# Kernel tuning notes

Hardware: AMD Instinct MI355X
Metric: run time of the kernel (lower is better)

Reference implementation:

```python
import jax, jax.numpy as jnp
import numpy as np

N_NODES = 100000
N_EDGES = 1600000
N_GRAPHS = 64
IN_CH = 128
HID = 128
N_CLASSES = 8


def setup_inputs() -> dict:
    key = jax.random.key(0)
    ks = jax.random.split(key, 8)
    x = jax.random.normal(ks[0], (N_NODES, IN_CH), dtype=jnp.float32)
    edge_index = jax.random.randint(ks[1], (2, N_EDGES), 0, N_NODES, dtype=jnp.int64)
    batch = jnp.sort(jax.random.randint(ks[2], (N_NODES,), 0, N_GRAPHS, dtype=jnp.int64))
    s1 = 1.0 / np.sqrt(IN_CH)
    s2 = 1.0 / np.sqrt(HID)
    W1 = jax.random.normal(ks[3], (IN_CH, HID), dtype=jnp.float32) * s1
    b1 = jnp.zeros((HID,), dtype=jnp.float32)
    W2 = jax.random.normal(ks[4], (HID, HID), dtype=jnp.float32) * s2
    b2 = jnp.zeros((HID,), dtype=jnp.float32)
    lin_W = jax.random.normal(ks[5], (HID, N_CLASSES), dtype=jnp.float32) * s2
    lin_b = jnp.zeros((N_CLASSES,), dtype=jnp.float32)
    return {"x": x, "edge_index": edge_index, "batch": batch,
            "W1": W1, "b1": b1, "W2": W2, "b2": b2,
            "lin_W": lin_W, "lin_b": lin_b}


def _gcn_norm(edge_index, n_nodes):
    # add self-loops, compute symmetric normalization coefficients
    loops = jnp.arange(n_nodes, dtype=edge_index.dtype)
    src = jnp.concatenate([edge_index[0], loops])
    dst = jnp.concatenate([edge_index[1], loops])
    ones = jnp.ones(src.shape[0], dtype=jnp.float32)
    deg = jax.ops.segment_sum(ones, dst, num_segments=n_nodes)
    dinv = jnp.where(deg > 0, jax.lax.rsqrt(jnp.maximum(deg, 1.0)), 0.0)
    norm = dinv[src] * dinv[dst]  # [E + N]
    return src, dst, norm


def _gcn_conv(x, W, b, src, dst, norm, n_nodes):
    xw = x @ W                               # [N, H]
    msg = xw[src] * norm[:, None]            # gather + scale, [E+N, H]
    out = jax.ops.segment_sum(msg, dst, num_segments=n_nodes)
    return out + b


def reference(x, edge_index, batch, W1, b1, W2, b2, lin_W, lin_b):
    n = x.shape[0]
    src, dst, norm = _gcn_norm(edge_index, n)
    h = jax.nn.relu(_gcn_conv(x, W1, b1, src, dst, norm, n))
    h = _gcn_conv(h, W2, b2, src, dst, norm, n)
    # global mean pool over graphs
    sums = jax.ops.segment_sum(h, batch, num_segments=N_GRAPHS)
    cnts = jax.ops.segment_sum(jnp.ones(n, dtype=h.dtype), batch, num_segments=N_GRAPHS)
    pooled = sums / jnp.maximum(cnts, 1.0)[:, None]
    return pooled @ lin_W + lin_b
```

## Files before the change

kernel.cpp:

```cpp
#include <hip/hip_runtime.h>
#include <hip/hip_fp16.h>
#include <cstdint>
#include <cstddef>

#define NNODES 100000
#define NEDGES 1600000
#define NGRAPHS 64
#define BSHIFT 7
#define BRANGE 128
#define NB 782
#define CAP 4096
#define NZ NB
#define LP 136
#define NAB 25000

typedef short short8v __attribute__((ext_vector_type(8)));
typedef float float4v __attribute__((ext_vector_type(4)));
typedef float float2v __attribute__((ext_vector_type(2)));

__device__ inline short f2h_s(float f) {
    __half h = __float2half(f);
    return __builtin_bit_cast(short, h);
}
__device__ inline ushort f2h_u(float f) {
    __half h = __float2half(f);
    return __builtin_bit_cast(ushort, h);
}
__device__ inline uint h22u(__half2 h) { return __builtin_bit_cast(uint, h); }

__device__ inline float2v fp8x2_f32(uint u) {
    return __builtin_amdgcn_cvt_pk_f32_fp8((int)u, false);
}
__device__ inline ushort f32_fp8x2(float a, float b) {
    return (ushort)__builtin_amdgcn_cvt_pk_fp8_f32(a, b, 0, false);
}


__global__ __launch_bounds__(256) void k_setup(int* __restrict__ zb,
                                               const float* __restrict__ W1,
                                               const float* __restrict__ W2,
                                               short8v* __restrict__ o1,
                                               short8v* __restrict__ o2,
                                               uint* __restrict__ rowNA,
                                               uint* __restrict__ rowNH,
                                               const int* __restrict__ batch,
                                               int* __restrict__ gstart,
                                               int* __restrict__ gend) {
    int b = blockIdx.x, t = threadIdx.x;
    if (b < 4) {
        int i = b * 256 + t;
        if (i < NZ) zb[i] = 0;
    } else if (b < 6) {
        const float* W = (b == 5) ? W2 : W1;
        short8v* o = (b == 5) ? o2 : o1;
        for (int s = t; s < 2048; s += 256) {
            int p = s >> 6, l = s & 63;
            int kb = (p >> 3) * 32 + ((l >> 4) * 8);
            int j = (p & 7) * 16 + (l & 15);
            short8v v;
            #pragma unroll
            for (int i = 0; i < 8; ++i)
                v[i] = f2h_s(W[(size_t)(kb + i) * 128 + j]);
            o[s] = v;
        }
    } else if (b == 6) {
        if (t < 32) rowNA[t] = 0u;
        else if (t < 64) rowNH[t - 32] = 0u;
    } else {
        int i = (b - 7) * 256 + t;
        if (i < NNODES) {
            int bb = batch[i];
            if (i == 0 || batch[i - 1] != bb) gstart[bb] = i;
            if (i == NNODES - 1 || batch[i + 1] != bb) gend[bb] = i + 1;
        }
    }
}


#define P1_EPT 16
__global__ __launch_bounds__(512) void k_bscatter(const int* __restrict__ src,
                                                  const int* __restrict__ dst,
                                                  int* __restrict__ bcur,
                                                  uint* __restrict__ pairs, int E) {
    __shared__ int h[NB];
    __shared__ int base[NB];
    int t = threadIdx.x;
    long long c0 = (long long)blockIdx.x * 8192;
    if (c0 >= E) return;
    for (int i = t; i < NB; i += 512) h[i] = 0;
    __syncthreads();
    int myb[P1_EPT], mylp[P1_EPT];
    uint myv[P1_EPT];
    #pragma unroll
    for (int k = 0; k < P1_EPT; ++k) {
        long long e = c0 + t + k * 512;
        if (e < E) {
            int d = dst[e];
            myv[k] = (uint)src[e] | ((uint)(d & (BRANGE - 1)) << 24);
            myb[k] = d >> BSHIFT;
            mylp[k] = atomicAdd(&h[myb[k]], 1);
        } else myb[k] = -1;
    }
    __syncthreads();
    for (int i = t; i < NB; i += 512)
        base[i] = h[i] ? atomicAdd(&bcur[i], h[i]) : 0;
    __syncthreads();
    #pragma unroll
    for (int k = 0; k < P1_EPT; ++k)
        if (myb[k] >= 0) {
            int pos = base[myb[k]] + mylp[k];
            if (pos < CAP)
                pairs[(size_t)myb[k] * CAP + pos] = myv[k];
        }
}


__global__ __launch_bounds__(512) void k_build(const uint* __restrict__ pairs,
                                               const int* __restrict__ bcur,
                                               int2* __restrict__ nr,
                                               float* __restrict__ dinv,
                                               int* __restrict__ csr, int N) {
    __shared__ int h[256];
    __shared__ int sh[256];
    __shared__ int cur[BRANGE];
    __shared__ int pend[BRANGE];
    int b = blockIdx.x, t = threadIdx.x;
    if (t < 256) h[t] = 0;
    __syncthreads();
    const int p0 = b * CAP;
    const int cntb = min(bcur[b], CAP);
    for (int p = t; p < cntb; p += 512)
        atomicAdd(&h[pairs[p0 + p] >> 24], 1);
    __syncthreads();
    int myh = (t < 256) ? h[t] : 0;
    int p8 = (myh + 7) & ~7;
    if (t < 256) sh[t] = p8;
    __syncthreads();
    #pragma unroll
    for (int d = 1; d < 256; d <<= 1) {
        int val = (t >= d && t < 256) ? sh[t - d] : 0;
        __syncthreads();
        if (t < 256) sh[t] += val;
        __syncthreads();
    }
    int node = (b << BSHIFT) + t;
    if (t < BRANGE) {
        int st = p0 + sh[t] - p8;
        cur[t] = st;
        pend[t] = st + p8;
        if (node < N) {
            nr[node] = make_int2(st, st + p8);
            dinv[node] = rsqrtf((float)(myh + 1));
        }
    }
    __syncthreads();
    for (int p = t; p < cntb; p += 512) {
        uint pr = pairs[p0 + p];
        int pos = atomicAdd(&cur[pr >> 24], 1);
        csr[pos] = (int)(pr & 0x00FFFFFFu);
    }
    __syncthreads();
    if (t < BRANGE) {
        for (int pos = cur[t]; pos < pend[t]; ++pos)
            csr[pos] = N;
    }
}


__global__ __launch_bounds__(256) void k_gemm_f32(const float4* __restrict__ X4,
                                                  const short8v* __restrict__ wf,
                                                  const float* __restrict__ dinv,
                                                  ushort* __restrict__ Y8, int n) {
    __shared__ ushort ht[16 * LP];
    const int t = threadIdx.x;
    const int lane = t & 63;
    const int w = t >> 6;
    const int row0 = blockIdx.x * 16;

    #pragma unroll
    for (int s = t; s < 16 * 32; s += 256) {
        int row = s >> 5, q = s & 31;
        float4 v = X4[(size_t)(row0 + row) * 32 + q];
        ushort2 h0 = make_ushort2(f2h_u(v.x), f2h_u(v.y));
        ushort2 h1 = make_ushort2(f2h_u(v.z), f2h_u(v.w));
        *(ushort2*)&ht[row * LP + q * 4] = h0;
        *(ushort2*)&ht[row * LP + q * 4 + 2] = h1;
    }
    __syncthreads();

    float4v acc[2];
    acc[0] = (float4v)0.f;
    acc[1] = (float4v)0.f;
    const int arow = lane & 15;
    const int ct0 = w * 2;
    #pragma unroll
    for (int kk = 0; kk < 4; ++kk) {
        short8v a = *(const short8v*)&ht[arow * LP + kk * 32 + ((lane >> 4) * 8)];
        acc[0] = __builtin_amdgcn_mfma_f32_16x16x32_f16(a, wf[(kk * 8 + ct0) * 64 + lane],
                                                        acc[0], 0, 0, 0);
        acc[1] = __builtin_amdgcn_mfma_f32_16x16x32_f16(a, wf[(kk * 8 + ct0 + 1) * 64 + lane],
                                                        acc[1], 0, 0, 0);
    }
    const int orow = row0 + ((lane >> 4) << 2);
    #pragma unroll
    for (int r = 0; r < 4; ++r) {
        int row = orow + r;
        float dr = dinv[row];
        #pragma unroll
        for (int j = 0; j < 2; ++j) {
            float a = acc[j][r] * dr;
            float b = __shfl_xor(a, 1);
            if (!(lane & 1))
                Y8[(size_t)row * 64 + (ct0 + j) * 8 + ((lane & 15) >> 1)] = f32_fp8x2(a, b);
        }
    }
}


__device__ inline void agg_node(const ushort* __restrict__ msg,
                                const int* __restrict__ csr,
                                int e0, int e1, int lane, uint uself,
                                float& outx, float& outy) {
    float2v a0 = fp8x2_f32(uself);
    float2v a1 = (float2v)0.f, a2 = (float2v)0.f, a3 = (float2v)0.f;
    for (int e = e0; e < e1; e += 64) {
        int me = e + lane;
        int sidx = (me < e1) ? csr[me] : NNODES;
        int cnt = min(64, e1 - e);
        for (int kb = 0; kb < cnt; kb += 8) {
            int s0 = __shfl(sidx, kb + 0);
            int s1 = __shfl(sidx, kb + 1);
            int s2 = __shfl(sidx, kb + 2);
            int s3 = __shfl(sidx, kb + 3);
            int s4 = __shfl(sidx, kb + 4);
            int s5 = __shfl(sidx, kb + 5);
            int s6 = __shfl(sidx, kb + 6);
            int s7 = __shfl(sidx, kb + 7);
            uint u0 = msg[(size_t)s0 * 64 + lane];
            uint u1 = msg[(size_t)s1 * 64 + lane];
            uint u2 = msg[(size_t)s2 * 64 + lane];
            uint u3 = msg[(size_t)s3 * 64 + lane];
            uint u4 = msg[(size_t)s4 * 64 + lane];
            uint u5 = msg[(size_t)s5 * 64 + lane];
            uint u6 = msg[(size_t)s6 * 64 + lane];
            uint u7 = msg[(size_t)s7 * 64 + lane];
            a0 += fp8x2_f32(u0);
            a1 += fp8x2_f32(u1);
            a2 += fp8x2_f32(u2);
            a3 += fp8x2_f32(u3);
            a0 += fp8x2_f32(u4);
            a1 += fp8x2_f32(u5);
            a2 += fp8x2_f32(u6);
            a3 += fp8x2_f32(u7);
        }
    }
    float2v s = (a0 + a1) + (a2 + a3);
    outx = s[0];
    outy = s[1];
}


__global__ __launch_bounds__(512) void k_agg_gemm(const ushort* __restrict__ msg,
                                                  const float* __restrict__ dinv,
                                                  const int2* __restrict__ nr,
                                                  const int* __restrict__ csr,
                                                  const float* __restrict__ bias,
                                                  const short8v* __restrict__ wf,
                                                  ushort* __restrict__ Y8, int n) {
    __shared__ ushort ht[16 * LP];
    const int t = threadIdx.x;
    const int lane = t & 63;
    const int w = t >> 6;
    const int row0 = blockIdx.x * 16;
    const float bx = bias[lane * 2];
    const float by = bias[lane * 2 + 1];

    #pragma unroll
    for (int i = 0; i < 2; ++i) {
        const int r = w * 2 + i;
        const int wid = row0 + r;
        const int2 rg = nr[wid];
        uint uself = msg[(size_t)wid * 64 + lane];
        float sx, sy;
        agg_node(msg, csr, rg.x, rg.y, lane, uself, sx, sy);
        float dd = dinv[wid];
        float ax = fmaxf(sx * dd + bx, 0.f);
        float ay = fmaxf(sy * dd + by, 0.f);
        *(uint*)&ht[r * LP + lane * 2] = h22u(__floats2half2_rn(ax, ay));
    }
    __syncthreads();

    float4v acc = (float4v)0.f;
    const int arow = lane & 15;
    #pragma unroll
    for (int kk = 0; kk < 4; ++kk) {
        short8v a = *(const short8v*)&ht[arow * LP + kk * 32 + ((lane >> 4) * 8)];
        acc = __builtin_amdgcn_mfma_f32_16x16x32_f16(a, wf[(kk * 8 + w) * 64 + lane],
                                                     acc, 0, 0, 0);
    }
    const int orow = row0 + ((lane >> 4) << 2);
    #pragma unroll
    for (int r = 0; r < 4; ++r) {
        int row = orow + r;
        float dr = dinv[row];
        float a = acc[r] * dr;
        float b = __shfl_xor(a, 1);
        if (!(lane & 1))
            Y8[(size_t)row * 64 + w * 8 + ((lane & 15) >> 1)] = f32_fp8x2(a, b);
    }
}


__global__ __launch_bounds__(256) void k_agg_pool(const ushort* __restrict__ msg,
                                                  const float* __restrict__ dinv,
                                                  const int2* __restrict__ nr,
                                                  const int* __restrict__ csr,
                                                  const int* __restrict__ batch,
                                                  float* __restrict__ pA,
                                                  float* __restrict__ pB) {
    __shared__ float red[4][128];
    __shared__ int selw[4];
    const int blk = blockIdx.x;
    const int t = threadIdx.x;
    const int lane = t & 63;
    const int w = t >> 6;
    const int wid = blk * 4 + w;

    const int2 rg = nr[wid];
    uint uself = msg[(size_t)wid * 64 + lane];
    float sx, sy;
    agg_node(msg, csr, rg.x, rg.y, lane, uself, sx, sy);
    float dd = dinv[wid];
    red[w][lane * 2] = sx * dd;
    red[w][lane * 2 + 1] = sy * dd;
    if (lane == 0) selw[w] = (batch[wid] != batch[blk * 4]) ? 1 : 0;
    __syncthreads();
    if (t < 128) {
        float a = 0.f, b = 0.f;
        #pragma unroll
        for (int ww = 0; ww < 4; ++ww) {
            float v = red[ww][t];
            if (selw[ww]) b += v; else a += v;
        }
        pA[(size_t)blk * 128 + t] = a;
        if (selw[0] | selw[1] | selw[2] | selw[3])
            pB[(size_t)blk * 128 + t] = b;
    }
}


__global__ __launch_bounds__(512) void k_final(const float* __restrict__ pA,
                                               const float* __restrict__ pB,
                                               const int* __restrict__ batch,
                                               const int* __restrict__ gstart,
                                               const int* __restrict__ gend,
                                               const float* __restrict__ b2,
                                               const float* __restrict__ linW,
                                               const float* __restrict__ linb,
                                               float* __restrict__ out) {
    __shared__ float sq[4][128];
    __shared__ float red[128][8];
    int g = blockIdx.x;
    int t = threadIdx.x;
    int c = t & 127;
    int q = t >> 7;
    int b0 = gstart[g] >> 2;
    int b1 = (gend[g] - 1) >> 2;
    float v = 0.f;
    #pragma unroll 4
    for (int b = b0 + 1 + q; b <= b1; b += 4)
        v += pA[(size_t)b * 128 + c];
    if (q == 0)
        v += ((batch[b0 * 4] != g) ? pB : pA)[(size_t)b0 * 128 + c];
    sq[q][c] = v;
    __syncthreads();
    if (t < 128) {
        float sv = sq[0][t] + sq[1][t] + sq[2][t] + sq[3][t];
        float cnt = (float)(gend[g] - gstart[g]);
        sv = sv / fmaxf(cnt, 1.0f) + b2[t];
        #pragma unroll
        for (int k = 0; k < 8; ++k) red[t][k] = sv * linW[(size_t)t * 8 + k];
    }
    __syncthreads();
    #pragma unroll
    for (int st = 64; st > 0; st >>= 1) {
        if (t < st) {
            #pragma unroll
            for (int k = 0; k < 8; ++k) red[t][k] += red[t + st][k];
        }
        __syncthreads();
    }
    if (t < 8) out[(size_t)g * 8 + t] = red[0][t] + linb[t];
}


extern "C" void kernel_launch(void* const* d_in, const int* in_sizes, int n_in,
                              void* d_out, int out_size, void* d_ws, size_t ws_size,
                              hipStream_t stream) {
    const float* x     = (const float*)d_in[0];
    const int*   ei    = (const int*)d_in[1];
    const int*   batch = (const int*)d_in[2];
    const float* W1    = (const float*)d_in[3];
    const float* b1    = (const float*)d_in[4];
    const float* W2    = (const float*)d_in[5];
    const float* b2    = (const float*)d_in[6];
    const float* linW  = (const float*)d_in[7];
    const float* linb  = (const float*)d_in[8];
    float* out = (float*)d_out;

    const int N = NNODES, E = NEDGES;
    const int* src = ei;
    const int* dst = ei + E;

    char* ws = (char*)d_ws;
    ushort* msgA8 = (ushort*)ws;   ws += (size_t)(N + 1) * 128;
    ushort* msgH8 = (ushort*)ws;   ws += (size_t)(N + 1) * 128;
    float* dinv   = (float*)ws;    ws += (size_t)N * 4;
    int2*  nr     = (int2*)ws;     ws += (size_t)N * 8;
    int*   csr    = (int*)ws;      ws += (size_t)NB * CAP * 4;
    uint*  pairs  = (uint*)ws;     ws += (size_t)NB * CAP * 4;
    int*   bcur   = (int*)ws;      ws += NB * 4;
    int*   gstart = (int*)ws;      ws += NGRAPHS * 4;
    int*   gend   = (int*)ws;      ws += NGRAPHS * 4;
    short8v* wf1  = (short8v*)ws;  ws += 2048 * 16;
    short8v* wf2  = (short8v*)ws;  ws += 2048 * 16;
    float* pA     = (float*)ws;    ws += (size_t)NAB * 128 * 4;
    float* pB     = (float*)ws;    ws += (size_t)NAB * 128 * 4;

    const int B = 256;

    k_setup<<<398, B, 0, stream>>>(bcur, W1, W2, wf1, wf2,
                                   (uint*)(msgA8 + (size_t)N * 64),
                                   (uint*)(msgH8 + (size_t)N * 64),
                                   batch, gstart, gend);

    k_bscatter<<<(E + 8191) / 8192, 512, 0, stream>>>(src, dst, bcur, pairs, E);
    k_build<<<NB, 512, 0, stream>>>(pairs, bcur, nr, dinv, csr, N);

    k_gemm_f32<<<N / 16, B, 0, stream>>>((const float4*)x, wf1, dinv, msgA8, N);

    k_agg_gemm<<<N / 16, 512, 0, stream>>>(msgA8, dinv, nr, csr, b1, wf2, msgH8, N);

    k_agg_pool<<<NAB, B, 0, stream>>>(msgH8, dinv, nr, csr, batch, pA, pB);

    k_final<<<NGRAPHS, 512, 0, stream>>>(pA, pB, batch, gstart, gend, b2, linW, linb, out);
}
```

Measured before the change: 168.1 us.

## Fold setup into scatter kernel and pool 16 nodes per block

Removes the separate setup kernel. Bucket-counter zeroing now goes through a memset, and weight conversion plus graph-boundary detection become extra blocks of the scatter kernel, which saves one launch. The aggregation+pool kernel now handles 16 nodes per 512-thread block instead of 4 per 256-thread block, which cuts partial-sum writes and the final reduction reads by four. In exchange there are fewer blocks, and each wave does two serial node aggregations.

```diff
diff --git a/kernel.cpp b/kernel.cpp
--- a/kernel.cpp
+++ b/kernel.cpp
@@ -10,9 +10,10 @@
 #define BRANGE 128
 #define NB 782
 #define CAP 4096
-#define NZ NB
 #define LP 136
-#define NAB 25000
+#define NSCAT 196
+#define NBND 196
+#define NPB 6250
 
 typedef short short8v __attribute__((ext_vector_type(8)));
 typedef float float4v __attribute__((ext_vector_type(4)));
@@ -33,47 +34,6 @@
 }
 __device__ inline ushort f32_fp8x2(float a, float b) {
     return (ushort)__builtin_amdgcn_cvt_pk_fp8_f32(a, b, 0, false);
-}
-
-
-__global__ __launch_bounds__(256) void k_setup(int* __restrict__ zb,
-                                               const float* __restrict__ W1,
-                                               const float* __restrict__ W2,
-                                               short8v* __restrict__ o1,
-                                               short8v* __restrict__ o2,
-                                               uint* __restrict__ rowNA,
-                                               uint* __restrict__ rowNH,
-                                               const int* __restrict__ batch,
-                                               int* __restrict__ gstart,
-                                               int* __restrict__ gend) {
-    int b = blockIdx.x, t = threadIdx.x;
-    if (b < 4) {
-        int i = b * 256 + t;
-        if (i < NZ) zb[i] = 0;
-    } else if (b < 6) {
-        const float* W = (b == 5) ? W2 : W1;
-        short8v* o = (b == 5) ? o2 : o1;
-        for (int s = t; s < 2048; s += 256) {
-            int p = s >> 6, l = s & 63;
-            int kb = (p >> 3) * 32 + ((l >> 4) * 8);
-            int j = (p & 7) * 16 + (l & 15);
-            short8v v;
-            #pragma unroll
-            for (int i = 0; i < 8; ++i)
-                v[i] = f2h_s(W[(size_t)(kb + i) * 128 + j]);
-            o[s] = v;
-        }
-    } else if (b == 6) {
-        if (t < 32) rowNA[t] = 0u;
-        else if (t < 64) rowNH[t - 32] = 0u;
-    } else {
-        int i = (b - 7) * 256 + t;
-        if (i < NNODES) {
-            int bb = batch[i];
-            if (i == 0 || batch[i - 1] != bb) gstart[bb] = i;
-            if (i == NNODES - 1 || batch[i + 1] != bb) gend[bb] = i + 1;
-        }
-    }
 }
 
 
@@ -81,12 +41,48 @@
 __global__ __launch_bounds__(512) void k_bscatter(const int* __restrict__ src,
                                                   const int* __restrict__ dst,
                                                   int* __restrict__ bcur,
-                                                  uint* __restrict__ pairs, int E) {
+                                                  uint* __restrict__ pairs,
+                                                  const float* __restrict__ W1,
+                                                  const float* __restrict__ W2,
+                                                  short8v* __restrict__ o1,
+                                                  short8v* __restrict__ o2,
+                                                  uint* __restrict__ rowNA,
+                                                  uint* __restrict__ rowNH,
+                                                  const int* __restrict__ batch,
+                                                  int* __restrict__ gstart,
+                                                  int* __restrict__ gend, int E) {
+    int b = blockIdx.x;
+    int t = threadIdx.x;
+    if (b >= NSCAT) {
+        if (b < NSCAT + 2) {
+            const float* W = (b == NSCAT + 1) ? W2 : W1;
+            short8v* o = (b == NSCAT + 1) ? o2 : o1;
+            for (int s = t; s < 2048; s += 512) {
+                int p = s >> 6, l = s & 63;
+                int kb = (p >> 3) * 32 + ((l >> 4) * 8);
+                int j = (p & 7) * 16 + (l & 15);
+                short8v v;
+                #pragma unroll
+                for (int i = 0; i < 8; ++i)
+                    v[i] = f2h_s(W[(size_t)(kb + i) * 128 + j]);
+                o[s] = v;
+            }
+        } else if (b == NSCAT + 2) {
+            if (t < 32) rowNA[t] = 0u;
+            else if (t < 64) rowNH[t - 32] = 0u;
+        } else {
+            int i = (b - (NSCAT + 3)) * 512 + t;
+            if (i < NNODES) {
+                int bb = batch[i];
+                if (i == 0 || batch[i - 1] != bb) gstart[bb] = i;
+                if (i == NNODES - 1 || batch[i + 1] != bb) gend[bb] = i + 1;
+            }
+        }
+        return;
+    }
     __shared__ int h[NB];
     __shared__ int base[NB];
-    int t = threadIdx.x;
-    long long c0 = (long long)blockIdx.x * 8192;
-    if (c0 >= E) return;
+    long long c0 = (long long)b * 8192;
     for (int i = t; i < NB; i += 512) h[i] = 0;
     __syncthreads();
     int myb[P1_EPT], mylp[P1_EPT];
@@ -311,39 +307,46 @@
 }
 
 
-__global__ __launch_bounds__(256) void k_agg_pool(const ushort* __restrict__ msg,
+__global__ __launch_bounds__(512) void k_agg_pool(const ushort* __restrict__ msg,
                                                   const float* __restrict__ dinv,
                                                   const int2* __restrict__ nr,
                                                   const int* __restrict__ csr,
                                                   const int* __restrict__ batch,
                                                   float* __restrict__ pA,
                                                   float* __restrict__ pB) {
-    __shared__ float red[4][128];
-    __shared__ int selw[4];
+    __shared__ float red[16][128];
+    __shared__ int selw[16];
     const int blk = blockIdx.x;
     const int t = threadIdx.x;
     const int lane = t & 63;
     const int w = t >> 6;
-    const int wid = blk * 4 + w;
-
-    const int2 rg = nr[wid];
-    uint uself = msg[(size_t)wid * 64 + lane];
-    float sx, sy;
-    agg_node(msg, csr, rg.x, rg.y, lane, uself, sx, sy);
-    float dd = dinv[wid];
-    red[w][lane * 2] = sx * dd;
-    red[w][lane * 2 + 1] = sy * dd;
-    if (lane == 0) selw[w] = (batch[wid] != batch[blk * 4]) ? 1 : 0;
+    const int node0 = blk * 16;
+
+    #pragma unroll
+    for (int i = 0; i < 2; ++i) {
+        const int r = w * 2 + i;
+        const int wid = node0 + r;
+        const int2 rg = nr[wid];
+        uint uself = msg[(size_t)wid * 64 + lane];
+        float sx, sy;
+        agg_node(msg, csr, rg.x, rg.y, lane, uself, sx, sy);
+        float dd = dinv[wid];
+        red[r][lane * 2] = sx * dd;
+        red[r][lane * 2 + 1] = sy * dd;
+        if (lane == 0) selw[r] = (batch[wid] != batch[node0]) ? 1 : 0;
+    }
     __syncthreads();
     if (t < 128) {
         float a = 0.f, b = 0.f;
+        int any = 0;
         #pragma unroll
-        for (int ww = 0; ww < 4; ++ww) {
+        for (int ww = 0; ww < 16; ++ww) {
             float v = red[ww][t];
             if (selw[ww]) b += v; else a += v;
+            any |= selw[ww];
         }
         pA[(size_t)blk * 128 + t] = a;
-        if (selw[0] | selw[1] | selw[2] | selw[3])
+        if (any)
             pB[(size_t)blk * 128 + t] = b;
     }
 }
@@ -364,14 +367,13 @@
     int t = threadIdx.x;
     int c = t & 127;
     int q = t >> 7;
-    int b0 = gstart[g] >> 2;
-    int b1 = (gend[g] - 1) >> 2;
+    int b0 = gstart[g] >> 4;
+    int b1 = (gend[g] - 1) >> 4;
     float v = 0.f;
-    #pragma unroll 4
     for (int b = b0 + 1 + q; b <= b1; b += 4)
         v += pA[(size_t)b * 128 + c];
     if (q == 0)
-        v += ((batch[b0 * 4] != g) ? pB : pA)[(size_t)b0 * 128 + c];
+        v += ((batch[b0 * 16] != g) ? pB : pA)[(size_t)b0 * 128 + c];
     sq[q][c] = v;
     __syncthreads();
     if (t < 128) {
@@ -424,24 +426,24 @@
     int*   gend   = (int*)ws;      ws += NGRAPHS * 4;
     short8v* wf1  = (short8v*)ws;  ws += 2048 * 16;
     short8v* wf2  = (short8v*)ws;  ws += 2048 * 16;
-    float* pA     = (float*)ws;    ws += (size_t)NAB * 128 * 4;
-    float* pB     = (float*)ws;    ws += (size_t)NAB * 128 * 4;
-
-    const int B = 256;
-
-    k_setup<<<398, B, 0, stream>>>(bcur, W1, W2, wf1, wf2,
-                                   (uint*)(msgA8 + (size_t)N * 64),
-                                   (uint*)(msgH8 + (size_t)N * 64),
-                                   batch, gstart, gend);
-
-    k_bscatter<<<(E + 8191) / 8192, 512, 0, stream>>>(src, dst, bcur, pairs, E);
+    float* pA     = (float*)ws;    ws += (size_t)NPB * 128 * 4;
+    float* pB     = (float*)ws;    ws += (size_t)NPB * 128 * 4;
+
+    hipMemsetAsync(bcur, 0, NB * sizeof(int), stream);
+
+    k_bscatter<<<NSCAT + 3 + NBND, 512, 0, stream>>>(src, dst, bcur, pairs,
+                                                     W1, W2, wf1, wf2,
+                                                     (uint*)(msgA8 + (size_t)N * 64),
+                                                     (uint*)(msgH8 + (size_t)N * 64),
+                                                     batch, gstart, gend, E);
+
     k_build<<<NB, 512, 0, stream>>>(pairs, bcur, nr, dinv, csr, N);
 
-    k_gemm_f32<<<N / 16, B, 0, stream>>>((const float4*)x, wf1, dinv, msgA8, N);
+    k_gemm_f32<<<N / 16, 256, 0, stream>>>((const float4*)x, wf1, dinv, msgA8, N);
 
     k_agg_gemm<<<N / 16, 512, 0, stream>>>(msgA8, dinv, nr, csr, b1, wf2, msgH8, N);
 
-    k_agg_pool<<<NAB, B, 0, stream>>>(msgH8, dinv, nr, csr, batch, pA, pB);
+    k_agg_pool<<<NPB, 512, 0, stream>>>(msgH8, dinv, nr, csr, batch, pA, pB);
 
     k_final<<<NGRAPHS, 512, 0, stream>>>(pA, pB, batch, gstart, gend, b2, linW, linb, out);
 }
```

Measured after the change: 167.5 us. Within noise of the previous version (-0.4%).
